# Optimization experiments

Hardware: AMD Instinct MI355X
Metric: run time of the kernel (lower is better)

Reference implementation:

```python
import jax, jax.numpy as jnp
import numpy as np
import math

N = 12288
IN_MAIN, IN_MOD = 64, 128
NC_INNER, NC_QK, OUT_MAIN = 16, 8, 64

def setup_inputs() -> dict:
    key = jax.random.key(0)
    ks = jax.random.split(key, 8)
    s = lambda fan_in: 1.0 / np.sqrt(fan_in)
    return {
        "x_main": jax.random.normal(ks[0], (N, IN_MAIN), dtype=jnp.float32),
        "x_mod": jax.random.normal(ks[1], (N, IN_MOD), dtype=jnp.float32),
        "xyz": jax.random.uniform(ks[2], (N, 3), dtype=jnp.float32),
        # MLP E: [in_main+in_mod -> nc_inner -> nc_inner], bias=False (weights stored [in, out])
        "W_e1": jax.random.uniform(ks[3], (IN_MAIN + IN_MOD, NC_INNER), jnp.float32, -s(IN_MAIN + IN_MOD), s(IN_MAIN + IN_MOD)),
        "W_e2": jax.random.uniform(ks[4], (NC_INNER, NC_INNER), jnp.float32, -s(NC_INNER), s(NC_INNER)),
        "W_q": jax.random.uniform(ks[5], (NC_INNER, NC_QK), jnp.float32, -s(NC_INNER), s(NC_INNER)),
        "W_k": jax.random.uniform(ks[6], (NC_INNER, NC_QK), jnp.float32, -s(NC_INNER), s(NC_INNER)),
        "W_v": jax.random.uniform(ks[7], (NC_INNER, OUT_MAIN), jnp.float32, -s(NC_INNER), s(NC_INNER)),
    }

def reference(x_main, x_mod, xyz, W_e1, W_e2, W_q, W_k, W_v):
    # concat 3D + 2D features: [N, in_main+in_mod]
    x = jnp.concatenate((x_main, x_mod), axis=-1)
    # MLP E (bias-free Linear + ReLU per layer): [N, nc_inner]
    h = jax.nn.relu(jax.nn.relu(x @ W_e1) @ W_e2)
    Q = h @ W_q  # [N, nc_qk]
    K = h @ W_k  # [N, nc_qk]
    V = h @ W_v  # [N, out_main]
    scale = 1.0 / math.sqrt(NC_QK)
    scores = (Q @ K.T) * scale          # [N, N] full global attention
    attn = jax.nn.softmax(scores, axis=1)
    return attn @ V                     # [N, out_main]
```

## Files before the change

kernel.cpp:

```cpp
#include <hip/hip_runtime.h>
#include <stdint.h>


#define NN 12288

typedef float    f32x16 __attribute__((ext_vector_type(16)));
typedef short    s16x8  __attribute__((ext_vector_type(8)));
typedef unsigned short u16;

#define MFMA_32x32x16_BF16 __builtin_amdgcn_mfma_f32_32x32x16_bf16

#define OFF_QB   0u
#define OFF_VT   196608u
#define OFF_PO   2162688u

#define VMCNT(n) (0x0F70 | (n))

typedef __attribute__((address_space(3))) void lds_void_t;
typedef const __attribute__((address_space(1))) void gbl_void_t;
__device__ __forceinline__ void gld16(const void* g, void* l) {
    __builtin_amdgcn_global_load_lds((gbl_void_t*)g, (lds_void_t*)l, 16, 0, 0);
}

__device__ __forceinline__ float bf2f(u16 s) {
    union { unsigned int u; float f; } c; c.u = ((unsigned int)s) << 16; return c.f;
}
__device__ __forceinline__ u16 f2bf(float f) {
    union { float f; unsigned int u; } c; c.f = f;
    return (u16)((c.u + 0x8000u) >> 16);
}
__device__ __forceinline__ unsigned int pk2(float a, float b) {
    union { float f; unsigned int u; } ca, cb; ca.f = a; cb.f = b;
    return ((ca.u + 0x8000u) >> 16) | ((cb.u + 0x8000u) & 0xffff0000u);
}
__device__ __forceinline__ unsigned int pkbf(float a, float b) {
#if __has_builtin(__builtin_amdgcn_cvt_pk_bf16_f32)
    auto r = __builtin_amdgcn_cvt_pk_bf16_f32(a, b);
    union { decltype(r) v; unsigned int u; } c; c.v = r; return c.u;
#else
    return pk2(a, b);
#endif
}
__device__ __forceinline__ f32x16 zf16() {
    f32x16 z;
#pragma unroll
    for (int i = 0; i < 16; ++i) z[i] = 0.f;
    return z;
}
__device__ __forceinline__ s16x8 zs8() {
    s16x8 z;
#pragma unroll
    for (int i = 0; i < 8; ++i) z[i] = 0;
    return z;
}

union U8 { s16x8 v; unsigned int u[4]; };

__global__ __launch_bounds__(256) void k1_qkv(
    const void* __restrict__ xmain, const void* __restrict__ xmod,
    const void* __restrict__ we1, const void* __restrict__ we2,
    const void* __restrict__ wqp, const void* __restrict__ wkp,
    const void* __restrict__ wvp,
    u16* __restrict__ qb, u16* __restrict__ vt)
{
    __shared__ float wf[4608];
    __shared__ int   sflag;
    __shared__ float lh1[64][4][17];
    __shared__ float lh2[64][17];

    const int t = threadIdx.x;
    const int r = t >> 2;
    const int p = t & 3;
    const int row = blockIdx.x * 64 + r;

    if (t == 0) sflag = 0;
    __syncthreads();
    {
        float v = bf2f(((const u16*)xmod)[2 * t]);
        if (fabsf(v) > 16.f) atomicAdd(&sflag, 1);
    }
    __syncthreads();
    const int isf32 = (sflag > 8);

    const float SCL = 0.51006979f;
    if (isf32) {
        const float* a1 = (const float*)we1; const float* a2 = (const float*)we2;
        const float* aq = (const float*)wqp; const float* ak = (const float*)wkp;
        const float* av = (const float*)wvp;
        for (int i = t; i < 4608; i += 256) {
            if      (i < 3072) wf[i] = a1[i];
            else if (i < 3328) wf[i] = a2[i - 3072];
            else if (i < 3456) wf[i] = aq[i - 3328] * SCL;
            else if (i < 3584) wf[i] = ak[i - 3456];
            else               wf[i] = av[i - 3584];
        }
    } else {
        const u16* a1 = (const u16*)we1; const u16* a2 = (const u16*)we2;
        const u16* aq = (const u16*)wqp; const u16* ak = (const u16*)wkp;
        const u16* av = (const u16*)wvp;
        for (int i = t; i < 4608; i += 256) {
            if      (i < 3072) wf[i] = bf2f(a1[i]);
            else if (i < 3328) wf[i] = bf2f(a2[i - 3072]);
            else if (i < 3456) wf[i] = bf2f(aq[i - 3328]) * SCL;
            else if (i < 3584) wf[i] = bf2f(ak[i - 3456]);
            else               wf[i] = bf2f(av[i - 3584]);
        }
    }
    __syncthreads();

    const float* __restrict__ W1 = wf;
    const float* __restrict__ W2 = wf + 3072;
    const float* __restrict__ Wq = wf + 3328;
    const float* __restrict__ Wk = wf + 3456;
    const float* __restrict__ Wv = wf + 3584;

    float h1p[16];
#pragma unroll
    for (int o = 0; o < 16; ++o) h1p[o] = 0.f;

    if (isf32) {
#pragma unroll
        for (int cc = 0; cc < 12; ++cc) {
            const int c = p + cc * 4;
            float4 xv = (c < 16)
                ? ((const float4*)xmain)[(size_t)row * 16 + c]
                : ((const float4*)xmod)[(size_t)row * 32 + (c - 16)];
            float xs[4] = {xv.x, xv.y, xv.z, xv.w};
#pragma unroll
            for (int j = 0; j < 4; ++j) {
                const float* wr = W1 + (c * 4 + j) * 16;
#pragma unroll
                for (int o = 0; o < 16; ++o) h1p[o] += xs[j] * wr[o];
            }
        }
    } else {
#pragma unroll
        for (int cc = 0; cc < 12; ++cc) {
            const int c = p + cc * 4;
            uint2 xv = (c < 16)
                ? ((const uint2*)xmain)[(size_t)row * 16 + c]
                : ((const uint2*)xmod)[(size_t)row * 32 + (c - 16)];
            float xs[4] = { bf2f((u16)(xv.x & 0xffff)), bf2f((u16)(xv.x >> 16)),
                            bf2f((u16)(xv.y & 0xffff)), bf2f((u16)(xv.y >> 16)) };
#pragma unroll
            for (int j = 0; j < 4; ++j) {
                const float* wr = W1 + (c * 4 + j) * 16;
#pragma unroll
                for (int o = 0; o < 16; ++o) h1p[o] += xs[j] * wr[o];
            }
        }
    }
#pragma unroll
    for (int o = 0; o < 16; ++o) lh1[r][p][o] = h1p[o];
    __syncthreads();

    float h1[16];
#pragma unroll
    for (int o = 0; o < 16; ++o)
        h1[o] = fmaxf(lh1[r][0][o] + lh1[r][1][o] + lh1[r][2][o] + lh1[r][3][o], 0.f);

#pragma unroll
    for (int oo = 0; oo < 4; ++oo) {
        const int o = p * 4 + oo;
        float s = 0.f;
#pragma unroll
        for (int j = 0; j < 16; ++j) s += h1[j] * W2[j * 16 + o];
        lh2[r][o] = fmaxf(s, 0.f);
    }
    __syncthreads();

    float h2[16];
#pragma unroll
    for (int j = 0; j < 16; ++j) h2[j] = lh2[r][j];

    {
        float q0 = 0.f, q1 = 0.f, k0 = 0.f, k1 = 0.f;
        const int o = 2 * p;
#pragma unroll
        for (int j = 0; j < 16; ++j) {
            q0 += h2[j] * Wq[j * 8 + o];
            q1 += h2[j] * Wq[j * 8 + o + 1];
            k0 += h2[j] * Wk[j * 8 + o];
            k1 += h2[j] * Wk[j * 8 + o + 1];
        }
        ((unsigned int*)qb)[(size_t)row * 4 + p] = pk2(q0, q1);
        ((unsigned int*)vt)[(size_t)(row >> 6) * 2560 + 2304 +
                            (row & 63) * 4 + p] = pk2(k0, k1);
    }

    const int ch = row >> 6, tI = (row >> 5) & 1, kk = row & 31;
#pragma unroll
    for (int c16 = 0; c16 < 16; ++c16) {
        const int c = p * 16 + c16;
        float v = 0.f;
#pragma unroll
        for (int j = 0; j < 16; ++j) v += h2[j] * Wv[j * 64 + c];
        vt[(size_t)ch * 5120 + tI * 2304 + c * 36 + kk] = f2bf(v);
    }
}


__device__ __forceinline__ void tile_pv(
    const f32x16& S, const u16* __restrict__ base, int l31, int half,
    const s16x8& ones, f32x16& acc0, f32x16& acc1, f32x16& accl)
{
    float pr[16];
#pragma unroll
    for (int r = 0; r < 16; ++r) pr[r] = __builtin_amdgcn_exp2f(S[r]);

    U8 p0, p1;
#pragma unroll
    for (int i = 0; i < 4; ++i) {
        p0.u[i] = pkbf(pr[2 * i],     pr[2 * i + 1]);
        p1.u[i] = pkbf(pr[8 + 2 * i], pr[8 + 2 * i + 1]);
    }

    accl = MFMA_32x32x16_BF16(ones, p0.v, accl, 0, 0, 0);
    accl = MFMA_32x32x16_BF16(ones, p1.v, accl, 0, 0, 0);

    const u16* r0 = base + l31 * 36 + 4 * half;
    const u16* r1 = base + (32 + l31) * 36 + 4 * half;
    U8 va;
    uint2 x0, x1;
    x0 = *(const uint2*)(r0);       x1 = *(const uint2*)(r0 + 8);
    va.u[0] = x0.x; va.u[1] = x0.y; va.u[2] = x1.x; va.u[3] = x1.y;
    acc0 = MFMA_32x32x16_BF16(va.v, p0.v, acc0, 0, 0, 0);
    x0 = *(const uint2*)(r1);       x1 = *(const uint2*)(r1 + 8);
    va.u[0] = x0.x; va.u[1] = x0.y; va.u[2] = x1.x; va.u[3] = x1.y;
    acc1 = MFMA_32x32x16_BF16(va.v, p0.v, acc1, 0, 0, 0);
    x0 = *(const uint2*)(r0 + 16);  x1 = *(const uint2*)(r0 + 24);
    va.u[0] = x0.x; va.u[1] = x0.y; va.u[2] = x1.x; va.u[3] = x1.y;
    acc0 = MFMA_32x32x16_BF16(va.v, p1.v, acc0, 0, 0, 0);
    x0 = *(const uint2*)(r1 + 16);  x1 = *(const uint2*)(r1 + 24);
    va.u[0] = x0.x; va.u[1] = x0.y; va.u[2] = x1.x; va.u[3] = x1.y;
    acc1 = MFMA_32x32x16_BF16(va.v, p1.v, acc1, 0, 0, 0);
}

__device__ __forceinline__ void chunk_body(
    const u16* __restrict__ base, const s16x8& qf, const s16x8& ones,
    int l31, int half, f32x16& acc0, f32x16& acc1, f32x16& accl)
{
    const f32x16 Z = zf16();
    s16x8 ka0 = *(const s16x8*)(base + 4608 + l31 * 8);
    s16x8 ka1 = *(const s16x8*)(base + 4864 + l31 * 8);
    {
        f32x16 Sa = MFMA_32x32x16_BF16(ka0, qf, Z, 0, 0, 0);
        tile_pv(Sa, base, l31, half, ones, acc0, acc1, accl);
    }
    {
        f32x16 Sb = MFMA_32x32x16_BF16(ka1, qf, Z, 0, 0, 0);
        tile_pv(Sb, base + 2304, l31, half, ones, acc0, acc1, accl);
    }
}

__global__ __launch_bounds__(256, 4) void k2_attn(
    const u16* __restrict__ qb, const u16* __restrict__ vt,
    u16* __restrict__ po, float* __restrict__ pl,
    int nsplit, int niter)
{
    __shared__ union SM {
        uint4 stage[4][640];
        float sf[8712];
    } sm;

    const int tid  = threadIdx.x;
    const int lane = tid & 63;
    const int half = lane >> 5;
    const int l31  = lane & 31;
    const int w    = tid >> 6;
    const int qB   = (blockIdx.x % 96) * 128;
    const int sp   = blockIdx.x / 96;
    const int myq  = qB + 32 * w;
    const int key_start = sp * (NN / nsplit);
    const int ch0 = key_start >> 6;

    const f32x16 Z = zf16();
    s16x8 qf = zs8();
    if (!half) qf = *(const s16x8*)(qb + (size_t)(myq + l31) * 8);

    s16x8 ones;
#pragma unroll
    for (int i = 0; i < 8; ++i) ones[i] = (short)0x3F80;

    f32x16 acc0 = Z, acc1 = Z, accl = Z;

    auto STAGE = [&](int c, int b) {
        const char* g = (const char*)vt + (size_t)(ch0 + c) * 10240
                      + 2560 * w + lane * 16;
        char* l = (char*)&sm.stage[b][0] + 2560 * w;
        gld16(g, l);
        gld16(g + 1024, l + 1024);
        if (lane < 32) gld16(g + 2048, l + 2048);
    };

    STAGE(0, 0);
    STAGE(1, 1);
    STAGE(2, 2);

    int it = 0;
    for (; it + 2 < niter; ++it) {
        __builtin_amdgcn_sched_barrier(0);
        __builtin_amdgcn_s_waitcnt(VMCNT(6));
        __builtin_amdgcn_s_barrier();
        __builtin_amdgcn_sched_barrier(0);
        if (it + 3 < niter) STAGE(it + 3, (it + 3) & 3);
        chunk_body((const u16*)&sm.stage[it & 3][0], qf, ones,
                   l31, half, acc0, acc1, accl);
    }
    __builtin_amdgcn_sched_barrier(0);
    __builtin_amdgcn_s_waitcnt(VMCNT(3));
    __builtin_amdgcn_s_barrier();
    __builtin_amdgcn_sched_barrier(0);
    chunk_body((const u16*)&sm.stage[it & 3][0], qf, ones,
               l31, half, acc0, acc1, accl);
    ++it;
    __builtin_amdgcn_sched_barrier(0);
    __builtin_amdgcn_s_waitcnt(VMCNT(0));
    __builtin_amdgcn_s_barrier();
    __builtin_amdgcn_sched_barrier(0);
    chunk_body((const u16*)&sm.stage[it & 3][0], qf, ones,
               l31, half, acc0, acc1, accl);

    const float ls = accl[0];

    __syncthreads();
    float* sfw = sm.sf + w * 2178;
#pragma unroll
    for (int r = 0; r < 16; ++r) {
        const int c = (r & 3) + 8 * (r >> 2) + 4 * half;
        sfw[c * 33 + l31]        = acc0[r];
        sfw[(32 + c) * 33 + l31] = acc1[r];
    }
    if (lane < 32) sfw[2112 + l31] = ls;

    u16* poS = po + (size_t)sp * (NN * 64);
    const int lq  = lane >> 1;
    const int cb0 = (lane & 1) * 32;
    unsigned int u[16];
#pragma unroll
    for (int i = 0; i < 16; ++i)
        u[i] = pkbf(sfw[(cb0 + 2 * i) * 33 + lq],
                    sfw[(cb0 + 2 * i + 1) * 33 + lq]);
    u16* dst = poS + (size_t)(myq + lq) * 64 + cb0;
    *(uint4*)(dst)      = make_uint4(u[0],  u[1],  u[2],  u[3]);
    *(uint4*)(dst + 8)  = make_uint4(u[4],  u[5],  u[6],  u[7]);
    *(uint4*)(dst + 16) = make_uint4(u[8],  u[9],  u[10], u[11]);
    *(uint4*)(dst + 24) = make_uint4(u[12], u[13], u[14], u[15]);
    if (lane < 32)
        pl[(size_t)sp * NN + myq + l31] = sfw[2112 + l31];
}

__global__ __launch_bounds__(256) void k3_norm(
    const u16* __restrict__ po, const float* __restrict__ pl,
    float4* __restrict__ out, int nsplit)
{
    const int i = blockIdx.x * 256 + threadIdx.x;
    const int row = i >> 4;
    const int c0 = (i & 15) * 4;
    float l = 0.f;
    float o0 = 0.f, o1 = 0.f, o2 = 0.f, o3 = 0.f;
    for (int s = 0; s < nsplit; ++s) {
        l += pl[(size_t)s * NN + row];
        uint2 p = *(const uint2*)(po + (size_t)s * (NN * 64) +
                                  (size_t)row * 64 + c0);
        o0 += bf2f((u16)(p.x & 0xffff)); o1 += bf2f((u16)(p.x >> 16));
        o2 += bf2f((u16)(p.y & 0xffff)); o3 += bf2f((u16)(p.y >> 16));
    }
    const float rl = 1.0f / l;
    out[i] = make_float4(o0 * rl, o1 * rl, o2 * rl, o3 * rl);
}

extern "C" void kernel_launch(void* const* d_in, const int* in_sizes, int n_in,
                              void* d_out, int out_size, void* d_ws, size_t ws_size,
                              hipStream_t stream)
{
    const void* xmain = d_in[0];
    const void* xmod  = d_in[1];
    const void* we1   = d_in[3];
    const void* we2   = d_in[4];
    const void* wq    = d_in[5];
    const void* wk    = d_in[6];
    const void* wv    = d_in[7];

    char* ws = (char*)d_ws;
    u16*   qb   = (u16*)  (ws + OFF_QB);
    u16*   vt   = (u16*)  (ws + OFF_VT);

    int S = 1;
    for (int cand = 32; cand >= 1; cand >>= 1) {
        size_t need = (size_t)OFF_PO + (size_t)cand * (NN * 64 * 2) +
                      (size_t)cand * (NN * 4);
        if (ws_size >= need) { S = cand; break; }
    }
    u16*   po = (u16*)(ws + OFF_PO);
    float* pl = (float*)(ws + OFF_PO + (size_t)S * (NN * 64 * 2));
    const int niter = NN / (64 * S);

    k1_qkv<<<192, 256, 0, stream>>>(xmain, xmod, we1, we2, wq, wk, wv,
                                    qb, vt);
    k2_attn<<<96 * S, 256, 0, stream>>>(qb, vt, po, pl, S, niter);
    k3_norm<<<768, 256, 0, stream>>>(po, pl, (float4*)d_out, S);
}
```

Baseline: 140.6 us.

## Load pre-swizzled V/K fragments directly to registers, drop LDS staging

Result: faster. 127.1 us (-9.6%).

```diff
diff --git a/kernel.cpp b/kernel.cpp
--- a/kernel.cpp
+++ b/kernel.cpp
@@ -13,14 +13,6 @@
 #define OFF_QB   0u
 #define OFF_VT   196608u
 #define OFF_PO   2162688u
-
-#define VMCNT(n) (0x0F70 | (n))
-
-typedef __attribute__((address_space(3))) void lds_void_t;
-typedef const __attribute__((address_space(1))) void gbl_void_t;
-__device__ __forceinline__ void gld16(const void* g, void* l) {
-    __builtin_amdgcn_global_load_lds((gbl_void_t*)g, (lds_void_t*)l, 16, 0, 0);
-}
 
 __device__ __forceinline__ float bf2f(u16 s) {
     union { unsigned int u; float f; } c; c.u = ((unsigned int)s) << 16; return c.f;
@@ -55,6 +47,7 @@
 }
 
 union U8 { s16x8 v; unsigned int u[4]; };
+union QV { uint4 q; s16x8 v; };
 
 __global__ __launch_bounds__(256) void k1_qkv(
     const void* __restrict__ xmain, const void* __restrict__ xmod,
@@ -184,84 +177,35 @@
             k1 += h2[j] * Wk[j * 8 + o + 1];
         }
         ((unsigned int*)qb)[(size_t)row * 4 + p] = pk2(q0, q1);
-        ((unsigned int*)vt)[(size_t)(row >> 6) * 2560 + 2304 +
+        ((unsigned int*)vt)[(size_t)(row >> 6) * 2304 + 2048 +
                             (row & 63) * 4 + p] = pk2(k0, k1);
     }
 
-    const int ch = row >> 6, tI = (row >> 5) & 1, kk = row & 31;
-#pragma unroll
-    for (int c16 = 0; c16 < 16; ++c16) {
-        const int c = p * 16 + c16;
-        float v = 0.f;
-#pragma unroll
-        for (int j = 0; j < 16; ++j) v += h2[j] * Wv[j * 64 + c];
-        vt[(size_t)ch * 5120 + tI * 2304 + c * 36 + kk] = f2bf(v);
-    }
-}
-
-
-__device__ __forceinline__ void tile_pv(
-    const f32x16& S, const u16* __restrict__ base, int l31, int half,
-    const s16x8& ones, f32x16& acc0, f32x16& acc1, f32x16& accl)
-{
-    float pr[16];
-#pragma unroll
-    for (int r = 0; r < 16; ++r) pr[r] = __builtin_amdgcn_exp2f(S[r]);
-
-    U8 p0, p1;
-#pragma unroll
-    for (int i = 0; i < 4; ++i) {
-        p0.u[i] = pkbf(pr[2 * i],     pr[2 * i + 1]);
-        p1.u[i] = pkbf(pr[8 + 2 * i], pr[8 + 2 * i + 1]);
-    }
-
-    accl = MFMA_32x32x16_BF16(ones, p0.v, accl, 0, 0, 0);
-    accl = MFMA_32x32x16_BF16(ones, p1.v, accl, 0, 0, 0);
-
-    const u16* r0 = base + l31 * 36 + 4 * half;
-    const u16* r1 = base + (32 + l31) * 36 + 4 * half;
-    U8 va;
-    uint2 x0, x1;
-    x0 = *(const uint2*)(r0);       x1 = *(const uint2*)(r0 + 8);
-    va.u[0] = x0.x; va.u[1] = x0.y; va.u[2] = x1.x; va.u[3] = x1.y;
-    acc0 = MFMA_32x32x16_BF16(va.v, p0.v, acc0, 0, 0, 0);
-    x0 = *(const uint2*)(r1);       x1 = *(const uint2*)(r1 + 8);
-    va.u[0] = x0.x; va.u[1] = x0.y; va.u[2] = x1.x; va.u[3] = x1.y;
-    acc1 = MFMA_32x32x16_BF16(va.v, p0.v, acc1, 0, 0, 0);
-    x0 = *(const uint2*)(r0 + 16);  x1 = *(const uint2*)(r0 + 24);
-    va.u[0] = x0.x; va.u[1] = x0.y; va.u[2] = x1.x; va.u[3] = x1.y;
-    acc0 = MFMA_32x32x16_BF16(va.v, p1.v, acc0, 0, 0, 0);
-    x0 = *(const uint2*)(r1 + 16);  x1 = *(const uint2*)(r1 + 24);
-    va.u[0] = x0.x; va.u[1] = x0.y; va.u[2] = x1.x; va.u[3] = x1.y;
-    acc1 = MFMA_32x32x16_BF16(va.v, p1.v, acc1, 0, 0, 0);
-}
-
-__device__ __forceinline__ void chunk_body(
-    const u16* __restrict__ base, const s16x8& qf, const s16x8& ones,
-    int l31, int half, f32x16& acc0, f32x16& acc1, f32x16& accl)
-{
-    const f32x16 Z = zf16();
-    s16x8 ka0 = *(const s16x8*)(base + 4608 + l31 * 8);
-    s16x8 ka1 = *(const s16x8*)(base + 4864 + l31 * 8);
     {
-        f32x16 Sa = MFMA_32x32x16_BF16(ka0, qf, Z, 0, 0, 0);
-        tile_pv(Sa, base, l31, half, ones, acc0, acc1, accl);
-    }
-    {
-        f32x16 Sb = MFMA_32x32x16_BF16(ka1, qf, Z, 0, 0, 0);
-        tile_pv(Sb, base + 2304, l31, half, ones, acc0, acc1, accl);
-    }
-}
-
-__global__ __launch_bounds__(256, 4) void k2_attn(
+        const int ch = row >> 6, tI = (row >> 5) & 1, kk = row & 31;
+        const int b   = kk >> 4, kk4 = kk & 15;
+        const int hh  = (kk4 >> 2) & 1;
+        const int jj  = (kk4 & 3) + 4 * (kk4 >> 3);
+        const size_t cbase = (size_t)ch * 4608 + (size_t)(tI * 4 + b) * 512
+                           + hh * 256 + jj;
+#pragma unroll
+        for (int c16 = 0; c16 < 16; ++c16) {
+            const int c = p * 16 + c16;
+            float v = 0.f;
+#pragma unroll
+            for (int j = 0; j < 16; ++j) v += h2[j] * Wv[j * 64 + c];
+            vt[cbase + (size_t)(c >> 5) * 1024 + (c & 31) * 8] = f2bf(v);
+        }
+    }
+}
+
+
+__global__ __launch_bounds__(256, 3) void k2_attn(
     const u16* __restrict__ qb, const u16* __restrict__ vt,
     u16* __restrict__ po, float* __restrict__ pl,
-    int nsplit, int niter)
+    int nsplit, int ntile)
 {
-    __shared__ union SM {
-        uint4 stage[4][640];
-        float sf[8712];
-    } sm;
+    __shared__ float sf[4][2178];
 
     const int tid  = threadIdx.x;
     const int lane = tid & 63;
@@ -272,7 +216,7 @@
     const int sp   = blockIdx.x / 96;
     const int myq  = qB + 32 * w;
     const int key_start = sp * (NN / nsplit);
-    const int ch0 = key_start >> 6;
+    const char* vbase = (const char*)vt + (size_t)(key_start >> 6) * 9216;
 
     const f32x16 Z = zf16();
     s16x8 qf = zs8();
@@ -284,47 +228,56 @@
 
     f32x16 acc0 = Z, acc1 = Z, accl = Z;
 
-    auto STAGE = [&](int c, int b) {
-        const char* g = (const char*)vt + (size_t)(ch0 + c) * 10240
-                      + 2560 * w + lane * 16;
-        char* l = (char*)&sm.stage[b][0] + 2560 * w;
-        gld16(g, l);
-        gld16(g + 1024, l + 1024);
-        if (lane < 32) gld16(g + 2048, l + 2048);
-    };
-
-    STAGE(0, 0);
-    STAGE(1, 1);
-    STAGE(2, 2);
-
-    int it = 0;
-    for (; it + 2 < niter; ++it) {
-        __builtin_amdgcn_sched_barrier(0);
-        __builtin_amdgcn_s_waitcnt(VMCNT(6));
-        __builtin_amdgcn_s_barrier();
-        __builtin_amdgcn_sched_barrier(0);
-        if (it + 3 < niter) STAGE(it + 3, (it + 3) & 3);
-        chunk_body((const u16*)&sm.stage[it & 3][0], qf, ones,
-                   l31, half, acc0, acc1, accl);
-    }
-    __builtin_amdgcn_sched_barrier(0);
-    __builtin_amdgcn_s_waitcnt(VMCNT(3));
-    __builtin_amdgcn_s_barrier();
-    __builtin_amdgcn_sched_barrier(0);
-    chunk_body((const u16*)&sm.stage[it & 3][0], qf, ones,
-               l31, half, acc0, acc1, accl);
-    ++it;
-    __builtin_amdgcn_sched_barrier(0);
-    __builtin_amdgcn_s_waitcnt(VMCNT(0));
-    __builtin_amdgcn_s_barrier();
-    __builtin_amdgcn_sched_barrier(0);
-    chunk_body((const u16*)&sm.stage[it & 3][0], qf, ones,
-               l31, half, acc0, acc1, accl);
+    QV kaA, f00A, f10A, f01A, f11A;
+    QV kaB, f00B, f10B, f01B, f11B;
+
+#define LDT(gt, ka, f00, f10, f01, f11) do {                                  \
+    const char* cb_ = vbase + (size_t)((gt) >> 1) * 9216 + ((gt) & 1) * 4096; \
+    (f00).q = *(const uint4*)(cb_ +        lane * 16);                        \
+    (f01).q = *(const uint4*)(cb_ + 1024 + lane * 16);                        \
+    (f10).q = *(const uint4*)(cb_ + 2048 + lane * 16);                        \
+    (f11).q = *(const uint4*)(cb_ + 3072 + lane * 16);                        \
+    (ka).q  = *(const uint4*)(vbase + (size_t)((gt) >> 1) * 9216 + 8192       \
+                              + ((gt) & 1) * 512 + l31 * 16);                 \
+} while (0)
+
+#define TILE(ka, f00, f10, f01, f11) do {                                     \
+    f32x16 S_ = MFMA_32x32x16_BF16((ka).v, qf, Z, 0, 0, 0);                   \
+    float pr_[16];                                                            \
+    _Pragma("unroll")                                                         \
+    for (int r_ = 0; r_ < 16; ++r_) pr_[r_] = __builtin_amdgcn_exp2f(S_[r_]); \
+    U8 p0_, p1_;                                                              \
+    _Pragma("unroll")                                                         \
+    for (int i_ = 0; i_ < 4; ++i_) {                                          \
+        p0_.u[i_] = pkbf(pr_[2 * i_],     pr_[2 * i_ + 1]);                   \
+        p1_.u[i_] = pkbf(pr_[8 + 2 * i_], pr_[8 + 2 * i_ + 1]);               \
+    }                                                                         \
+    accl = MFMA_32x32x16_BF16(ones, p0_.v, accl, 0, 0, 0);                    \
+    accl = MFMA_32x32x16_BF16(ones, p1_.v, accl, 0, 0, 0);                    \
+    acc0 = MFMA_32x32x16_BF16((f00).v, p0_.v, acc0, 0, 0, 0);                 \
+    acc1 = MFMA_32x32x16_BF16((f10).v, p0_.v, acc1, 0, 0, 0);                 \
+    acc0 = MFMA_32x32x16_BF16((f01).v, p1_.v, acc0, 0, 0, 0);                 \
+    acc1 = MFMA_32x32x16_BF16((f11).v, p1_.v, acc1, 0, 0, 0);                 \
+} while (0)
+
+    LDT(0, kaA, f00A, f10A, f01A, f11A);
+    int gt = 0;
+    for (; gt + 2 < ntile; gt += 2) {
+        LDT(gt + 1, kaB, f00B, f10B, f01B, f11B);
+        TILE(kaA, f00A, f10A, f01A, f11A);
+        LDT(gt + 2, kaA, f00A, f10A, f01A, f11A);
+        TILE(kaB, f00B, f10B, f01B, f11B);
+    }
+    LDT(gt + 1, kaB, f00B, f10B, f01B, f11B);
+    TILE(kaA, f00A, f10A, f01A, f11A);
+    TILE(kaB, f00B, f10B, f01B, f11B);
+
+#undef LDT
+#undef TILE
 
     const float ls = accl[0];
 
-    __syncthreads();
-    float* sfw = sm.sf + w * 2178;
+    float* sfw = &sf[w][0];
 #pragma unroll
     for (int r = 0; r < 16; ++r) {
         const int c = (r & 3) + 8 * (r >> 2) + 4 * half;
@@ -386,18 +339,19 @@
     u16*   qb   = (u16*)  (ws + OFF_QB);
     u16*   vt   = (u16*)  (ws + OFF_VT);
 
-    int S = 1;
-    for (int cand = 32; cand >= 1; cand >>= 1) {
-        size_t need = (size_t)OFF_PO + (size_t)cand * (NN * 64 * 2) +
-                      (size_t)cand * (NN * 4);
-        if (ws_size >= need) { S = cand; break; }
+    int S = 8;
+    while (S > 1) {
+        size_t need = (size_t)OFF_PO + (size_t)S * (NN * 64 * 2) +
+                      (size_t)S * (NN * 4);
+        if (ws_size >= need) break;
+        S >>= 1;
     }
     u16*   po = (u16*)(ws + OFF_PO);
     float* pl = (float*)(ws + OFF_PO + (size_t)S * (NN * 64 * 2));
-    const int niter = NN / (64 * S);
+    const int ntile = NN / (32 * S);
 
     k1_qkv<<<192, 256, 0, stream>>>(xmain, xmod, we1, we2, wq, wk, wv,
                                     qb, vt);
-    k2_attn<<<96 * S, 256, 0, stream>>>(qb, vt, po, pl, S, niter);
+    k2_attn<<<96 * S, 256, 0, stream>>>(qb, vt, po, pl, S, ntile);
     k3_norm<<<768, 256, 0, stream>>>(po, pl, (float4*)d_out, S);
 }
```
